# Performance work log

Hardware: AMD Instinct MI355X
Metric: run time of the kernel (lower is better)

## Reference

```python
import jax, jax.numpy as jnp
import numpy as np

EPS = 1e-12

def _dist(a, b):
    # euclidean distance between matching vectors along last axis,
    # computed exactly as pdist_torch: ||a||^2 + ||b||^2 - 2 a.b, clamp, sqrt
    sq = jnp.sum(a * a, -1) + jnp.sum(b * b, -1) - 2.0 * jnp.sum(a * b, -1)
    return jnp.sqrt(jnp.clip(sq, EPS))


def setup_inputs() -> dict:
    key = jax.random.key(0)
    k1, k2 = jax.random.split(key)
    N, D = 8192, 2048
    input1 = jax.random.normal(k1, (N, D), dtype=jnp.float32)
    input2 = jax.random.normal(k2, (N, D), dtype=jnp.float32)
    return {"input1": input1, "input2": input2, "num_pos": 4}


def reference(input1, input2, num_pos):
    N, D = input1.shape
    id_num = N // num_pos
    r = input1.reshape(id_num, num_pos, D)   # RGB features per identity
    ir = input2.reshape(id_num, num_pos, D)  # IR features per identity

    cross_center_rgb = jnp.mean(r, axis=1)   # [id_num, D]
    cross_center_ir = jnpp = jnp.mean(ir, axis=1)

    # leave-one-out intra centers (vectorized): (sum - x) / (num_pos - 1)
    loo_rgb = (jnp.sum(r, axis=1, keepdims=True) - r) / (num_pos - 1)  # [id,pos,D]
    # NOTE: faithful to original bug — intra IR center is also built from RGB feats
    loo_ir = loo_rgb

    d_intra_rgb = _dist(r, loo_rgb)                        # [id, pos]
    d_intra_ir = _dist(ir, loo_ir)
    d_cross_rgb = _dist(r, cross_center_ir[:, None, :])
    d_cross_ir = _dist(ir, cross_center_rgb[:, None, :])

    loss = jnp.sum((d_cross_rgb - d_intra_rgb) ** 2
                   + (d_cross_ir - d_intra_ir) ** 2) / N / 2.0
    return loss
```

## Files before the change

### kernel.cpp

```cpp
#include <hip/hip_runtime.h>
#include <hip/hip_bf16.h>


constexpr int D    = 2048;
constexpr int NPOS = 4;
constexpr int TPB  = 256;
constexpr int VEC4 = D / 4;
constexpr int ITER = VEC4 / TPB;
constexpr int NACC = 25;

__global__ void zero_out_kernel(float* out) { out[0] = 0.0f; }

__global__ void __launch_bounds__(TPB) msel_feat_kernel(
        const float* __restrict__ in1,
        const float* __restrict__ in2,
        float* __restrict__ out) {
    const long id = blockIdx.x;
    const float* __restrict__ ra = in1 + id * (long)(NPOS * D);
    const float* __restrict__ rb = in2 + id * (long)(NPOS * D);

    float acc[NACC];
#pragma unroll
    for (int k = 0; k < NACC; ++k) acc[k] = 0.0f;

#pragma unroll
    for (int it = 0; it < ITER; ++it) {
        const int c = (threadIdx.x + it * TPB) * 4;
        float rv[NPOS][4], iv[NPOS][4];
#pragma unroll
        for (int p = 0; p < NPOS; ++p) {
            *reinterpret_cast<float4*>(&rv[p][0]) =
                *reinterpret_cast<const float4*>(ra + p * D + c);
            *reinterpret_cast<float4*>(&iv[p][0]) =
                *reinterpret_cast<const float4*>(rb + p * D + c);
        }
#pragma unroll
        for (int e = 0; e < 4; ++e) {
            const float s = rv[0][e] + rv[1][e] + rv[2][e] + rv[3][e];
            const float t = iv[0][e] + iv[1][e] + iv[2][e] + iv[3][e];
            acc[24] = fmaf(t, t, acc[24]);
#pragma unroll
            for (int p = 0; p < NPOS; ++p) {
                const float x = rv[p][e];
                const float y = iv[p][e];
                acc[0  + p] = fmaf(x, x, acc[0  + p]);
                acc[4  + p] = fmaf(y, y, acc[4  + p]);
                acc[8  + p] = fmaf(s, x, acc[8  + p]);
                acc[12 + p] = fmaf(s, y, acc[12 + p]);
                acc[16 + p] = fmaf(x, y, acc[16 + p]);
                acc[20 + p] = fmaf(x, t, acc[20 + p]);
            }
        }
    }

#pragma unroll
    for (int k = 0; k < NACC; ++k) {
        float v = acc[k];
#pragma unroll
        for (int off = 32; off > 0; off >>= 1) v += __shfl_down(v, off, 64);
        acc[k] = v;
    }

    __shared__ float lds[TPB / 64][NACC];
    const int wave = threadIdx.x >> 6;
    const int lane = threadIdx.x & 63;
    if (lane == 0) {
#pragma unroll
        for (int k = 0; k < NACC; ++k) lds[wave][k] = acc[k];
    }
    __syncthreads();

    if (threadIdx.x == 0) {
        float tot[NACC];
#pragma unroll
        for (int k = 0; k < NACC; ++k)
            tot[k] = lds[0][k] + lds[1][k] + lds[2][k] + lds[3][k];

        const float ss = tot[8] + tot[9] + tot[10] + tot[11];
        const float tt = tot[24];
        float contrib = 0.0f;
#pragma unroll
        for (int p = 0; p < NPOS; ++p) {
            const float rr = tot[0 + p];
            const float ii = tot[4 + p];
            const float sr = tot[8 + p];
            const float si = tot[12 + p];
            const float ri = tot[16 + p];
            const float rt = tot[20 + p];

            const float b2loo = (ss - 2.0f * sr + rr) * (1.0f / 9.0f);
            const float sq_intra_rgb = rr + b2loo - 2.0f * ((sr - rr) * (1.0f / 3.0f));
            const float sq_intra_ir  = ii + b2loo - 2.0f * ((si - ri) * (1.0f / 3.0f));
            const float sq_cross_rgb = rr + tt * 0.0625f - 0.5f * rt;
            const float sq_cross_ir  = ii + ss * 0.0625f - 0.5f * si;

            const float d_ir_rgb = sqrtf(fmaxf(sq_intra_rgb, 1e-12f));
            const float d_ir_ir  = sqrtf(fmaxf(sq_intra_ir,  1e-12f));
            const float d_cr_rgb = sqrtf(fmaxf(sq_cross_rgb, 1e-12f));
            const float d_cr_ir  = sqrtf(fmaxf(sq_cross_ir,  1e-12f));

            const float e1 = d_cr_rgb - d_ir_rgb;
            const float e2 = d_cr_ir  - d_ir_ir;
            contrib += e1 * e1 + e2 * e2;
        }
        atomicAdd(out, contrib * (1.0f / 16384.0f));
    }
}

extern "C" void kernel_launch(void* const* d_in, const int* in_sizes, int n_in,
                              void* d_out, int out_size, void* d_ws, size_t ws_size,
                              hipStream_t stream) {
    const float* in1 = (const float*)d_in[0];
    const float* in2 = (const float*)d_in[1];
    float* out = (float*)d_out;

    const int id_num = in_sizes[0] / (NPOS * D);

    zero_out_kernel<<<1, 1, 0, stream>>>(out);
    msel_feat_kernel<<<id_num, TPB, 0, stream>>>(in1, in2, out);
}
```

Before: 148.5 us.

## Split each identity across two blocks with workspace partials and an epilogue kernel

Each identity's feature dimension is split across two blocks, so twice as many blocks each do one float4 iteration per thread. The 25 partial dot products per identity are atomically accumulated into a workspace, and a separate epilogue kernel computes the distances and reduces the loss per block before a single atomic per block. This raises parallelism and spreads the many per-identity atomics on one output address over fewer operations. In exchange it adds a workspace memset, a second kernel launch, and 25 atomics per block into global memory.

```diff
diff --git a/kernel.cpp b/kernel.cpp
--- a/kernel.cpp
+++ b/kernel.cpp
@@ -5,51 +5,49 @@
 constexpr int D    = 2048;
 constexpr int NPOS = 4;
 constexpr int TPB  = 256;
-constexpr int VEC4 = D / 4;
-constexpr int ITER = VEC4 / TPB;
 constexpr int NACC = 25;
+constexpr int SPLIT = 2;
 
-__global__ void zero_out_kernel(float* out) { out[0] = 0.0f; }
-
-__global__ void __launch_bounds__(TPB) msel_feat_kernel(
+__global__ void __launch_bounds__(TPB) msel_partial_kernel(
         const float* __restrict__ in1,
         const float* __restrict__ in2,
-        float* __restrict__ out) {
-    const long id = blockIdx.x;
-    const float* __restrict__ ra = in1 + id * (long)(NPOS * D);
-    const float* __restrict__ rb = in2 + id * (long)(NPOS * D);
+        float* __restrict__ ws,
+        int id_num) {
+    const int b  = blockIdx.x;
+    const int id = b >> 1;
+    const int hf = b & 1;
+    const float* __restrict__ ra = in1 + (long)id * (NPOS * D);
+    const float* __restrict__ rb = in2 + (long)id * (NPOS * D);
+    const int c = (hf * TPB + threadIdx.x) * 4;
+
+    float rv[NPOS][4], iv[NPOS][4];
+#pragma unroll
+    for (int p = 0; p < NPOS; ++p) {
+        *reinterpret_cast<float4*>(&rv[p][0]) =
+            *reinterpret_cast<const float4*>(ra + p * D + c);
+        *reinterpret_cast<float4*>(&iv[p][0]) =
+            *reinterpret_cast<const float4*>(rb + p * D + c);
+    }
 
     float acc[NACC];
 #pragma unroll
     for (int k = 0; k < NACC; ++k) acc[k] = 0.0f;
 
 #pragma unroll
-    for (int it = 0; it < ITER; ++it) {
-        const int c = (threadIdx.x + it * TPB) * 4;
-        float rv[NPOS][4], iv[NPOS][4];
+    for (int e = 0; e < 4; ++e) {
+        const float s = rv[0][e] + rv[1][e] + rv[2][e] + rv[3][e];
+        const float t = iv[0][e] + iv[1][e] + iv[2][e] + iv[3][e];
+        acc[24] = fmaf(t, t, acc[24]);
 #pragma unroll
         for (int p = 0; p < NPOS; ++p) {
-            *reinterpret_cast<float4*>(&rv[p][0]) =
-                *reinterpret_cast<const float4*>(ra + p * D + c);
-            *reinterpret_cast<float4*>(&iv[p][0]) =
-                *reinterpret_cast<const float4*>(rb + p * D + c);
-        }
-#pragma unroll
-        for (int e = 0; e < 4; ++e) {
-            const float s = rv[0][e] + rv[1][e] + rv[2][e] + rv[3][e];
-            const float t = iv[0][e] + iv[1][e] + iv[2][e] + iv[3][e];
-            acc[24] = fmaf(t, t, acc[24]);
-#pragma unroll
-            for (int p = 0; p < NPOS; ++p) {
-                const float x = rv[p][e];
-                const float y = iv[p][e];
-                acc[0  + p] = fmaf(x, x, acc[0  + p]);
-                acc[4  + p] = fmaf(y, y, acc[4  + p]);
-                acc[8  + p] = fmaf(s, x, acc[8  + p]);
-                acc[12 + p] = fmaf(s, y, acc[12 + p]);
-                acc[16 + p] = fmaf(x, y, acc[16 + p]);
-                acc[20 + p] = fmaf(x, t, acc[20 + p]);
-            }
+            const float x = rv[p][e];
+            const float y = iv[p][e];
+            acc[0  + p] = fmaf(x, x, acc[0  + p]);
+            acc[4  + p] = fmaf(y, y, acc[4  + p]);
+            acc[8  + p] = fmaf(s, x, acc[8  + p]);
+            acc[12 + p] = fmaf(s, y, acc[12 + p]);
+            acc[16 + p] = fmaf(x, y, acc[16 + p]);
+            acc[20 + p] = fmaf(x, t, acc[20 + p]);
         }
     }
 
@@ -70,15 +68,24 @@
     }
     __syncthreads();
 
-    if (threadIdx.x == 0) {
+    if (threadIdx.x < NACC) {
+        const int k = threadIdx.x;
+        const float tot = lds[0][k] + lds[1][k] + lds[2][k] + lds[3][k];
+        atomicAdd(ws + k * id_num + id, tot);
+    }
+}
+
+__global__ void __launch_bounds__(TPB) msel_epilogue_kernel(
+        const float* __restrict__ ws, float* __restrict__ out, int id_num) {
+    const int id = blockIdx.x * TPB + threadIdx.x;
+    float contrib = 0.0f;
+    if (id < id_num) {
         float tot[NACC];
 #pragma unroll
-        for (int k = 0; k < NACC; ++k)
-            tot[k] = lds[0][k] + lds[1][k] + lds[2][k] + lds[3][k];
+        for (int k = 0; k < NACC; ++k) tot[k] = ws[k * id_num + id];
 
         const float ss = tot[8] + tot[9] + tot[10] + tot[11];
         const float tt = tot[24];
-        float contrib = 0.0f;
 #pragma unroll
         for (int p = 0; p < NPOS; ++p) {
             const float rr = tot[0 + p];
@@ -103,7 +110,18 @@
             const float e2 = d_cr_ir  - d_ir_ir;
             contrib += e1 * e1 + e2 * e2;
         }
-        atomicAdd(out, contrib * (1.0f / 16384.0f));
+        contrib *= (1.0f / 16384.0f);
+    }
+
+#pragma unroll
+    for (int off = 32; off > 0; off >>= 1) contrib += __shfl_down(contrib, off, 64);
+    __shared__ float lds[TPB / 64];
+    const int wave = threadIdx.x >> 6;
+    if ((threadIdx.x & 63) == 0) lds[wave] = contrib;
+    __syncthreads();
+    if (threadIdx.x == 0) {
+        float v = lds[0] + lds[1] + lds[2] + lds[3];
+        atomicAdd(out, v);
     }
 }
 
@@ -113,9 +131,13 @@
     const float* in1 = (const float*)d_in[0];
     const float* in2 = (const float*)d_in[1];
     float* out = (float*)d_out;
+    float* ws  = (float*)d_ws;
 
     const int id_num = in_sizes[0] / (NPOS * D);
 
-    zero_out_kernel<<<1, 1, 0, stream>>>(out);
-    msel_feat_kernel<<<id_num, TPB, 0, stream>>>(in1, in2, out);
+    hipMemsetAsync(ws, 0, (size_t)NACC * id_num * sizeof(float), stream);
+    hipMemsetAsync(out, 0, sizeof(float), stream);
+
+    msel_partial_kernel<<<id_num * SPLIT, TPB, 0, stream>>>(in1, in2, ws, id_num);
+    msel_epilogue_kernel<<<(id_num + TPB - 1) / TPB, TPB, 0, stream>>>(ws, out, id_num);
 }
```

Measured after the change: 157.6 us. +6.2%, slower.
